# Optimization experiments

Hardware: AMD Instinct MI355X
Metric: run time of the kernel (lower is better)

Reference implementation:

```python
import jax, jax.numpy as jnp
import numpy as np
import math

B, T, C = 2, 2048, 1024
H = 16            # n_head
RATIO = 4         # ratio_kv
HKV = H // RATIO  # n_head_kv = 4
HD = C // H       # head_dim = 64
G = H // HKV      # query heads per kv head = 4


def _alibi_slopes(n_heads):
    # n_heads must be a power of 2 here (H=16)
    assert math.log2(n_heads).is_integer()
    start = 2.0 ** (-(2.0 ** (-(math.log2(n_heads) - 3))))
    return np.array([start * (start ** i) for i in range(n_heads)], dtype=np.float32)


def setup_inputs() -> dict:
    key = jax.random.key(0)
    ks = jax.random.split(key, 5)
    return {
        "x": jax.random.normal(ks[0], (B, T, C), dtype=jnp.float32),
        "Wq": jax.random.normal(ks[1], (C, C), dtype=jnp.float32) * 0.02,
        "Wk": jax.random.normal(ks[2], (C, HKV * HD), dtype=jnp.float32) * 0.02,
        "Wv": jax.random.normal(ks[3], (C, HKV * HD), dtype=jnp.float32) * 0.02,
        "Wo": jax.random.normal(ks[4], (C, C), dtype=jnp.float32) * 0.02,
    }


def reference(x, Wq, Wk, Wv, Wo):
    # GQA causal attention with ALiBi bias (flash-disabled fallback path).
    # q: [B,HKV,G,T,HD] (grouped query heads), k/v: [B,HKV,T,HD]
    q = (x @ Wq).reshape(B, T, H, HD).transpose(0, 2, 1, 3).reshape(B, HKV, G, T, HD)
    k = (x @ Wk).reshape(B, T, HKV, HD).transpose(0, 2, 1, 3)
    v = (x @ Wv).reshape(B, T, HKV, HD).transpose(0, 2, 1, 3)

    scale = 1.0 / math.sqrt(HD)
    att = jnp.einsum('bkgtd,bksd->bkgts', q, k) * scale  # [B,HKV,G,T,T]

    # ALiBi: original repeats alibi(n_head) by G and truncates to n_head,
    # so query head h uses slope get_slopes(H)[h // G] == slopes[:HKV] per kv group.
    slopes = jnp.asarray(_alibi_slopes(H))[:HKV]          # [HKV]
    pos = jnp.arange(T)
    rel = (pos[None, :] - pos[:, None]).astype(jnp.float32)  # [T,T], rel[i,j]=j-i
    bias = slopes[:, None, None] * rel                    # [HKV,T,T]
    causal = jnp.triu(jnp.full((T, T), -jnp.inf, dtype=jnp.float32), 1)

    att = att + bias[None, :, None] + causal
    att = jax.nn.softmax(att.astype(jnp.float32), axis=-1).astype(q.dtype)

    y = jnp.einsum('bkgts,bksd->bkgtd', att, v)           # [B,HKV,G,T,HD]
    y = y.reshape(B, H, T, HD).transpose(0, 2, 1, 3).reshape(B, T, C)
    return y @ Wo
```

## Files before the change

kernel.cpp:

```cpp
#include <hip/hip_runtime.h>
#include <hip/hip_bf16.h>
#include <math.h>

#define B_ 2
#define T_ 2048
#define C_ 1024
#define H_ 16
#define HKV_ 4
#define G_ 4
#define HD_ 64
#define KVC_ 256
#define NQKV_ 1536
#define NQT_ 32

typedef __attribute__((ext_vector_type(8))) short bf16x8;
typedef __attribute__((ext_vector_type(4))) float f32x4;

static __device__ inline short f2bf(float f) {
    __hip_bfloat16 h = __float2bfloat16(f);
    short s;
    __builtin_memcpy(&s, &h, 2);
    return s;
}
static __device__ inline short f2bf_trunc(float f) {
    unsigned int u;
    __builtin_memcpy(&u, &f, 4);
    return (short)(u >> 16);
}
static __device__ inline float bf2f(short s) {
    unsigned int u = ((unsigned int)(unsigned short)s) << 16;
    float f;
    __builtin_memcpy(&f, &u, 4);
    return f;
}

static __device__ inline void gload_lds16(const short* g, short* lds) {
    __builtin_amdgcn_global_load_lds(
        (const __attribute__((address_space(1))) unsigned int*)g,
        (__attribute__((address_space(3))) unsigned int*)lds, 16, 0, 0);
}

__global__ __launch_bounds__(256) void cast_bf16(
    const float* __restrict__ in, short* __restrict__ out, int n)
{
    const int i = (blockIdx.x * 256 + threadIdx.x) * 8;
    if (i >= n) return;
    const float4 a = *(const float4*)(in + i);
    const float4 b = *(const float4*)(in + i + 4);
    bf16x8 o;
    o[0] = f2bf(a.x); o[1] = f2bf(a.y); o[2] = f2bf(a.z); o[3] = f2bf(a.w);
    o[4] = f2bf(b.x); o[5] = f2bf(b.y); o[6] = f2bf(b.z); o[7] = f2bf(b.w);
    *(bf16x8*)(out + i) = o;
}

__global__ __launch_bounds__(256) void w_transpose(
    const float* __restrict__ Wq, const float* __restrict__ Wk,
    const float* __restrict__ Wv, const float* __restrict__ Wo,
    short* __restrict__ Wt, short* __restrict__ Wot)
{
    const int z = blockIdx.z;
    const float* in;
    short* out;
    int N;
    if (z == 0)      { in = Wq; out = Wt;                     N = C_; }
    else if (z == 1) { in = Wk; out = Wt + C_ * C_;           N = KVC_; }
    else if (z == 2) { in = Wv; out = Wt + (C_ + KVC_) * C_;  N = KVC_; }
    else             { in = Wo; out = Wot;                    N = C_; }
    const int n0 = blockIdx.x * 32;
    if (n0 >= N) return;
    __shared__ float t[32][33];
    const int tx = threadIdx.x, ty = threadIdx.y;
    const int k0 = blockIdx.y * 32;
    #pragma unroll
    for (int j = 0; j < 4; j++)
        t[ty + j * 8][tx] = in[(size_t)(k0 + ty + j * 8) * N + n0 + tx];
    __syncthreads();
    #pragma unroll
    for (int j = 0; j < 4; j++)
        out[(size_t)(n0 + ty + j * 8) * C_ + k0 + tx] = f2bf(t[tx][ty + j * 8]);
}

template <bool OUT_BF16>
__global__ __launch_bounds__(256) void gemm_bf16(
    const short* __restrict__ A, const short* __restrict__ Bt,
    void* __restrict__ Cout, int M, int N, int K)
{
    __shared__ short As[64 * 32];
    __shared__ short Bs[128 * 32];
    const int tid = threadIdx.x;
    const int wave = tid >> 6, lane = tid & 63;
    const int l15 = lane & 15, quad = lane >> 4;
    const int row0 = blockIdx.y * 64, col0 = blockIdx.x * 128;
    const int wrow = (wave >> 1) * 32, wcol = (wave & 1) * 64;

    f32x4 acc[2][4];
    #pragma unroll
    for (int i = 0; i < 2; i++)
        #pragma unroll
        for (int j = 0; j < 4; j++)
            acc[i][j] = (f32x4){0.f, 0.f, 0.f, 0.f};

    for (int kt = 0; kt < K; kt += 32) {
        __syncthreads();
        {
            const int r = wave * 16 + (lane >> 2);
            const int kof = (lane & 3) * 8;
            gload_lds16(A + (size_t)(row0 + r) * K + kt + kof, &As[wave * 512]);
        }
        #pragma unroll
        for (int c2 = 0; c2 < 2; c2++) {
            const int c = wave * 2 + c2;
            const int r = c * 16 + (lane >> 2);
            const int kof = (lane & 3) * 8;
            gload_lds16(Bt + (size_t)(col0 + r) * K + kt + kof, &Bs[c * 512]);
        }
        __syncthreads();

        bf16x8 af[2], bf[4];
        #pragma unroll
        for (int mt = 0; mt < 2; mt++)
            af[mt] = *(const bf16x8*)&As[(wrow + mt * 16 + l15) * 32 + quad * 8];
        #pragma unroll
        for (int nt = 0; nt < 4; nt++)
            bf[nt] = *(const bf16x8*)&Bs[(wcol + nt * 16 + l15) * 32 + quad * 8];
        #pragma unroll
        for (int mt = 0; mt < 2; mt++)
            #pragma unroll
            for (int nt = 0; nt < 4; nt++)
                acc[mt][nt] = __builtin_amdgcn_mfma_f32_16x16x32_bf16(
                    af[mt], bf[nt], acc[mt][nt], 0, 0, 0);
    }

    #pragma unroll
    for (int mt = 0; mt < 2; mt++) {
        #pragma unroll
        for (int r = 0; r < 4; r++) {
            const size_t row = row0 + wrow + mt * 16 + quad * 4 + r;
            #pragma unroll
            for (int nt = 0; nt < 4; nt++) {
                const size_t col = col0 + wcol + nt * 16 + l15;
                if (OUT_BF16)
                    ((short*)Cout)[row * N + col] = f2bf(acc[mt][nt][r]);
                else
                    ((float*)Cout)[row * N + col] = acc[mt][nt][r];
            }
        }
    }
}

__global__ __launch_bounds__(256) void kv_tile(
    const short* __restrict__ QKV, short* __restrict__ Kt, short* __restrict__ Vt)
{
    __shared__ short Ls[64 * 72];
    const int jt = blockIdx.x;
    const int bk = blockIdx.y;
    const int b = bk >> 2, kh = bk & 3;
    const int tid = threadIdx.x;
    const int key = tid >> 2, d16 = (tid & 3) * 16;
    const size_t src = (size_t)(b * T_ + jt * 64 + key) * NQKV_ + C_ + kh * 64 + d16;
    const size_t tbase = (size_t)(bk * 32 + jt) * 4096;

    {
        const int db0 = (tid & 3) * 2, db1 = db0 + 1;
        *(bf16x8*)(Kt + tbase + key * 64 + ((db0 ^ (key & 7)) * 8)) =
            *(const bf16x8*)(QKV + src);
        *(bf16x8*)(Kt + tbase + key * 64 + ((db1 ^ (key & 7)) * 8)) =
            *(const bf16x8*)(QKV + src + 8);
    }
    *(bf16x8*)&Ls[key * 72 + d16]     = *(const bf16x8*)(QKV + src + KVC_);
    *(bf16x8*)&Ls[key * 72 + d16 + 8] = *(const bf16x8*)(QKV + src + KVC_ + 8);
    __syncthreads();
    const int d = tid >> 2, k16 = (tid & 3) * 16;
    bf16x8 o0, o1;
    #pragma unroll
    for (int i = 0; i < 8; i++) o0[i] = Ls[(k16 + i) * 72 + d];
    #pragma unroll
    for (int i = 0; i < 8; i++) o1[i] = Ls[(k16 + 8 + i) * 72 + d];
    const int kb0 = (tid & 3) * 2, kb1 = kb0 + 1;
    *(bf16x8*)(Vt + tbase + d * 64 + ((kb0 ^ (d & 7)) * 8)) = o0;
    *(bf16x8*)(Vt + tbase + d * 64 + ((kb1 ^ (d & 7)) * 8)) = o1;
}

#define LSTR 72

__global__ __launch_bounds__(256) void attn_mfma(
    const short* __restrict__ QKV, const short* __restrict__ Ktg,
    const short* __restrict__ Vtg, short* __restrict__ Y)
{
    const int qx = blockIdx.x;
    const int bh = blockIdx.y;
    const int qtL = qx, qtH = NQT_ - 1 - qx;
    const int b = bh >> 4, h = bh & 15, kh = h >> 2;
    const float slope2 = exp2f(-0.5f * (float)(kh + 1)) * 1.44269504f;
    const int tid = threadIdx.x;
    const int wave = tid >> 6, lane = tid & 63;
    const int l15 = lane & 15, quad = lane >> 4;
    const int lswz = (l15 & 7) * 8;

    __shared__ short Ks[4096];
    __shared__ short Vs[4096];
    __shared__ short Ps[4 * 32 * LSTR];
    short* Pw = &Ps[wave * 32 * LSTR];
    const int wswz = ((quad >> 1) & 1) << 4;
    const int rswz = ((l15 >> 3) & 1) << 4;

    const size_t bT = (size_t)b * T_;
    const size_t tb0 = (size_t)((b * HKV_ + kh) * 32) * 4096;
    const int qrow0H = qtH * 64 + wave * 16;
    const int qrow0L = qtL * 64 + wave * 16;

    const float qscale = 0.125f * 1.44269504f;
    bf16x8 qfH[2], qfL[2];
    #pragma unroll
    for (int k0 = 0; k0 < 2; k0++) {
        const short* qpH = QKV + (bT + qrow0H + l15) * NQKV_ + h * 64;
        const short* qpL = QKV + (bT + qrow0L + l15) * NQKV_ + h * 64;
        bf16x8 rH = *(const bf16x8*)(qpH + k0 * 32 + quad * 8);
        bf16x8 rL = *(const bf16x8*)(qpL + k0 * 32 + quad * 8);
        #pragma unroll
        for (int j = 0; j < 8; j++) {
            qfH[k0][j] = f2bf(bf2f(rH[j]) * qscale);
            qfL[k0][j] = f2bf(bf2f(rL[j]) * qscale);
        }
    }

    const short one_s = (short)0x3F80;
    const bf16x8 ones = {one_s, one_s, one_s, one_s, one_s, one_s, one_s, one_s};

    f32x4 OaccH[4], OaccL[4], laccH, laccL;
    #pragma unroll
    for (int nt = 0; nt < 4; nt++) {
        OaccH[nt] = (f32x4){0.f, 0.f, 0.f, 0.f};
        OaccL[nt] = (f32x4){0.f, 0.f, 0.f, 0.f};
    }
    laccH = (f32x4){0.f, 0.f, 0.f, 0.f};
    laccL = (f32x4){0.f, 0.f, 0.f, 0.f};

    for (int jtk = 0; jtk <= qtH; jtk++) {
        __syncthreads();
        {
            const short* Ktile = Ktg + tb0 + (size_t)jtk * 4096;
            const short* Vtile = Vtg + tb0 + (size_t)jtk * 4096;
            #pragma unroll
            for (int i = 0; i < 2; i++) {
                const int ch = wave * 2 + i;
                gload_lds16(Ktile + ch * 512 + lane * 8, &Ks[ch * 512]);
                gload_lds16(Vtile + ch * 512 + lane * 8, &Vs[ch * 512]);
            }
        }
        __syncthreads();

        const bool doL = (jtk <= qtL);

        bf16x8 kf[8];
        #pragma unroll
        for (int nt = 0; nt < 4; nt++)
            #pragma unroll
            for (int k0 = 0; k0 < 2; k0++)
                kf[nt * 2 + k0] = *(const bf16x8*)
                    &Ks[(nt * 16 + l15) * 64 + (((k0 * 4 + quad) * 8) ^ lswz)];

        f32x4 sH[4], sL[4];
        #pragma unroll
        for (int nt = 0; nt < 4; nt++) {
            f32x4 a = {0.f, 0.f, 0.f, 0.f};
            a = __builtin_amdgcn_mfma_f32_16x16x32_bf16(qfH[0], kf[nt*2+0], a, 0, 0, 0);
            a = __builtin_amdgcn_mfma_f32_16x16x32_bf16(qfH[1], kf[nt*2+1], a, 0, 0, 0);
            sH[nt] = a;
        }
        if (doL) {
            #pragma unroll
            for (int nt = 0; nt < 4; nt++) {
                f32x4 a = {0.f, 0.f, 0.f, 0.f};
                a = __builtin_amdgcn_mfma_f32_16x16x32_bf16(qfL[0], kf[nt*2+0], a, 0, 0, 0);
                a = __builtin_amdgcn_mfma_f32_16x16x32_bf16(qfL[1], kf[nt*2+1], a, 0, 0, 0);
                sL[nt] = a;
            }
        }

        {
            const float base = slope2 * (float)(jtk * 64 + l15 - quad * 4 - qrow0H);
            if (jtk == qtH) {
                #pragma unroll
                for (int nt = 0; nt < 4; nt++) {
                    const int colsw = ((nt * 16 + l15) ^ wswz);
                    #pragma unroll
                    for (int r = 0; r < 4; r++) {
                        const float relv = (float)(jtk * 64 + l15 - quad * 4 - qrow0H)
                                         + (float)(nt * 16 - r);
                        float p = __builtin_amdgcn_exp2f(
                            fmaf(slope2, (float)(nt * 16 - r), base) + sH[nt][r]);
                        if (relv > 0.f) p = 0.f;
                        Pw[(quad * 4 + r) * LSTR + colsw] = f2bf_trunc(p);
                    }
                }
            } else {
                #pragma unroll
                for (int nt = 0; nt < 4; nt++) {
                    const int colsw = ((nt * 16 + l15) ^ wswz);
                    #pragma unroll
                    for (int r = 0; r < 4; r++) {
                        float p = __builtin_amdgcn_exp2f(
                            fmaf(slope2, (float)(nt * 16 - r), base) + sH[nt][r]);
                        Pw[(quad * 4 + r) * LSTR + colsw] = f2bf_trunc(p);
                    }
                }
            }
        }
        if (doL) {
            const float base = slope2 * (float)(jtk * 64 + l15 - quad * 4 - qrow0L);
            if (jtk == qtL) {
                #pragma unroll
                for (int nt = 0; nt < 4; nt++) {
                    const int colsw = ((nt * 16 + l15) ^ wswz);
                    #pragma unroll
                    for (int r = 0; r < 4; r++) {
                        const float relv = (float)(jtk * 64 + l15 - quad * 4 - qrow0L)
                                         + (float)(nt * 16 - r);
                        float p = __builtin_amdgcn_exp2f(
                            fmaf(slope2, (float)(nt * 16 - r), base) + sL[nt][r]);
                        if (relv > 0.f) p = 0.f;
                        Pw[(16 + quad * 4 + r) * LSTR + colsw] = f2bf_trunc(p);
                    }
                }
            } else {
                #pragma unroll
                for (int nt = 0; nt < 4; nt++) {
                    const int colsw = ((nt * 16 + l15) ^ wswz);
                    #pragma unroll
                    for (int r = 0; r < 4; r++) {
                        float p = __builtin_amdgcn_exp2f(
                            fmaf(slope2, (float)(nt * 16 - r), base) + sL[nt][r]);
                        Pw[(16 + quad * 4 + r) * LSTR + colsw] = f2bf_trunc(p);
                    }
                }
            }
        }
        __asm__ volatile("s_waitcnt lgkmcnt(0)" ::: "memory");

        bf16x8 vf[8];
        #pragma unroll
        for (int nt = 0; nt < 4; nt++)
            #pragma unroll
            for (int k0 = 0; k0 < 2; k0++)
                vf[nt * 2 + k0] = *(const bf16x8*)
                    &Vs[(nt * 16 + l15) * 64 + (((k0 * 4 + quad) * 8) ^ lswz)];

        {
            bf16x8 pf0 = *(const bf16x8*)&Pw[l15 * LSTR + ((quad * 8) ^ rswz)];
            bf16x8 pf1 = *(const bf16x8*)&Pw[l15 * LSTR + ((32 + quad * 8) ^ rswz)];
            laccH = __builtin_amdgcn_mfma_f32_16x16x32_bf16(pf0, ones, laccH, 0, 0, 0);
            laccH = __builtin_amdgcn_mfma_f32_16x16x32_bf16(pf1, ones, laccH, 0, 0, 0);
            #pragma unroll
            for (int nt = 0; nt < 4; nt++) {
                OaccH[nt] = __builtin_amdgcn_mfma_f32_16x16x32_bf16(
                    pf0, vf[nt*2+0], OaccH[nt], 0, 0, 0);
                OaccH[nt] = __builtin_amdgcn_mfma_f32_16x16x32_bf16(
                    pf1, vf[nt*2+1], OaccH[nt], 0, 0, 0);
            }
        }
        if (doL) {
            bf16x8 pf0 = *(const bf16x8*)&Pw[(16 + l15) * LSTR + ((quad * 8) ^ rswz)];
            bf16x8 pf1 = *(const bf16x8*)&Pw[(16 + l15) * LSTR + ((32 + quad * 8) ^ rswz)];
            laccL = __builtin_amdgcn_mfma_f32_16x16x32_bf16(pf0, ones, laccL, 0, 0, 0);
            laccL = __builtin_amdgcn_mfma_f32_16x16x32_bf16(pf1, ones, laccL, 0, 0, 0);
            #pragma unroll
            for (int nt = 0; nt < 4; nt++) {
                OaccL[nt] = __builtin_amdgcn_mfma_f32_16x16x32_bf16(
                    pf0, vf[nt*2+0], OaccL[nt], 0, 0, 0);
                OaccL[nt] = __builtin_amdgcn_mfma_f32_16x16x32_bf16(
                    pf1, vf[nt*2+1], OaccL[nt], 0, 0, 0);
            }
        }
    }

    #pragma unroll
    for (int r = 0; r < 4; r++) {
        const float invH = 1.f / laccH[r];
        const float invL = 1.f / laccL[r];
        const int rowH = qrow0H + quad * 4 + r;
        const int rowL = qrow0L + quad * 4 + r;
        short* ypH = Y + (bT + rowH) * C_ + h * 64 + l15;
        short* ypL = Y + (bT + rowL) * C_ + h * 64 + l15;
        #pragma unroll
        for (int nt = 0; nt < 4; nt++) {
            ypH[nt * 16] = f2bf(OaccH[nt][r] * invH);
            ypL[nt * 16] = f2bf(OaccL[nt][r] * invL);
        }
    }
}

extern "C" void kernel_launch(void* const* d_in, const int* in_sizes, int n_in,
                              void* d_out, int out_size, void* d_ws, size_t ws_size,
                              hipStream_t stream) {
    const float* x  = (const float*)d_in[0];
    const float* Wq = (const float*)d_in[1];
    const float* Wk = (const float*)d_in[2];
    const float* Wv = (const float*)d_in[3];
    const float* Wo = (const float*)d_in[4];
    float* out = (float*)d_out;

    const int M = B_ * T_;
    short* xb  = (short*)d_ws;
    short* Wt  = xb  + (size_t)M * C_;
    short* Wot = Wt  + (size_t)NQKV_ * C_;
    short* QKV = Wot + (size_t)C_ * C_;
    short* Yb  = QKV + (size_t)M * NQKV_;
    short* Ktg = Yb  + (size_t)M * C_;
    short* Vtg = Ktg + (size_t)8 * 32 * 4096;

    cast_bf16<<<dim3(M * C_ / (256 * 8)), dim3(256), 0, stream>>>(x, xb, M * C_);
    w_transpose<<<dim3(32, 32, 4), dim3(32, 8), 0, stream>>>(Wq, Wk, Wv, Wo, Wt, Wot);

    gemm_bf16<true><<<dim3(NQKV_ / 128, M / 64), dim3(256), 0, stream>>>(
        xb, Wt, QKV, M, NQKV_, C_);
    kv_tile<<<dim3(32, 8), dim3(256), 0, stream>>>(QKV, Ktg, Vtg);
    attn_mfma<<<dim3(NQT_ / 2, B_ * H_), dim3(256), 0, stream>>>(QKV, Ktg, Vtg, Yb);
    gemm_bf16<false><<<dim3(C_ / 128, M / 64), dim3(256), 0, stream>>>(
        Yb, Wot, out, M, C_, C_);
}
```

Baseline: 176.1 us.

## Fuse K/V tiling into QKV GEMM epilogue and keep P in registers

The QKV GEMM epilogue now writes K and V directly into the swizzled per-tile layouts the attention kernel expects, which removes the separate kv_tile kernel and its extra global round trip. In attention, scores are computed transposed (K·Q) with the ALiBi bias preloaded into the accumulator. P is packed into bf16x4 registers and fed to 16x16x16 MFMAs for both the row sums and the PV product, so the LDS P staging buffer and its waits are gone. The trade is more MFMA instructions at half the K depth and scattered 2-byte stores for K in the GEMM epilogue.

Measured after the change: 190.9 us. +8.4%, slower.

```diff
diff --git a/kernel.cpp b/kernel.cpp
--- a/kernel.cpp
+++ b/kernel.cpp
@@ -14,6 +14,7 @@
 #define NQT_ 32
 
 typedef __attribute__((ext_vector_type(8))) short bf16x8;
+typedef __attribute__((ext_vector_type(4))) short bf16x4;
 typedef __attribute__((ext_vector_type(4))) float f32x4;
 
 static __device__ inline short f2bf(float f) {
@@ -22,16 +23,27 @@
     __builtin_memcpy(&s, &h, 2);
     return s;
 }
-static __device__ inline short f2bf_trunc(float f) {
-    unsigned int u;
-    __builtin_memcpy(&u, &f, 4);
-    return (short)(u >> 16);
-}
 static __device__ inline float bf2f(short s) {
     unsigned int u = ((unsigned int)(unsigned short)s) << 16;
     float f;
     __builtin_memcpy(&f, &u, 4);
     return f;
+}
+static __device__ inline bf16x4 pack4_trunc(float p0, float p1, float p2, float p3) {
+    unsigned a, b, c, d;
+    __builtin_memcpy(&a, &p0, 4); __builtin_memcpy(&b, &p1, 4);
+    __builtin_memcpy(&c, &p2, 4); __builtin_memcpy(&d, &p3, 4);
+    int2 v;
+    v.x = (int)((a >> 16) | (b & 0xffff0000u));
+    v.y = (int)((c >> 16) | (d & 0xffff0000u));
+    return __builtin_bit_cast(bf16x4, v);
+}
+
+static __device__ inline f32x4 mfma32(bf16x8 a, bf16x8 b, f32x4 c) {
+    return __builtin_amdgcn_mfma_f32_16x16x32_bf16(a, b, c, 0, 0, 0);
+}
+static __device__ inline f32x4 mfma16(bf16x4 a, bf16x4 b, f32x4 c) {
+    return __builtin_amdgcn_mfma_f32_16x16x16bf16_1k(a, b, c, 0, 0, 0);
 }
 
 static __device__ inline void gload_lds16(const short* g, short* lds) {
@@ -80,10 +92,11 @@
         out[(size_t)(n0 + ty + j * 8) * C_ + k0 + tx] = f2bf(t[tx][ty + j * 8]);
 }
 
-template <bool OUT_BF16>
+template <int MODE>
 __global__ __launch_bounds__(256) void gemm_bf16(
     const short* __restrict__ A, const short* __restrict__ Bt,
-    void* __restrict__ Cout, int M, int N, int K)
+    void* __restrict__ Cout, short* __restrict__ Ktg, short* __restrict__ Vtg,
+    int M, int N, int K)
 {
     __shared__ short As[64 * 32];
     __shared__ short Bs[128 * 32];
@@ -127,61 +140,68 @@
         for (int mt = 0; mt < 2; mt++)
             #pragma unroll
             for (int nt = 0; nt < 4; nt++)
-                acc[mt][nt] = __builtin_amdgcn_mfma_f32_16x16x32_bf16(
-                    af[mt], bf[nt], acc[mt][nt], 0, 0, 0);
-    }
-
-    #pragma unroll
-    for (int mt = 0; mt < 2; mt++) {
-        #pragma unroll
-        for (int r = 0; r < 4; r++) {
-            const size_t row = row0 + wrow + mt * 16 + quad * 4 + r;
-            #pragma unroll
-            for (int nt = 0; nt < 4; nt++) {
-                const size_t col = col0 + wcol + nt * 16 + l15;
-                if (OUT_BF16)
-                    ((short*)Cout)[row * N + col] = f2bf(acc[mt][nt][r]);
-                else
-                    ((float*)Cout)[row * N + col] = acc[mt][nt][r];
-            }
-        }
-    }
-}
-
-__global__ __launch_bounds__(256) void kv_tile(
-    const short* __restrict__ QKV, short* __restrict__ Kt, short* __restrict__ Vt)
-{
-    __shared__ short Ls[64 * 72];
-    const int jt = blockIdx.x;
-    const int bk = blockIdx.y;
-    const int b = bk >> 2, kh = bk & 3;
-    const int tid = threadIdx.x;
-    const int key = tid >> 2, d16 = (tid & 3) * 16;
-    const size_t src = (size_t)(b * T_ + jt * 64 + key) * NQKV_ + C_ + kh * 64 + d16;
-    const size_t tbase = (size_t)(bk * 32 + jt) * 4096;
-
-    {
-        const int db0 = (tid & 3) * 2, db1 = db0 + 1;
-        *(bf16x8*)(Kt + tbase + key * 64 + ((db0 ^ (key & 7)) * 8)) =
-            *(const bf16x8*)(QKV + src);
-        *(bf16x8*)(Kt + tbase + key * 64 + ((db1 ^ (key & 7)) * 8)) =
-            *(const bf16x8*)(QKV + src + 8);
-    }
-    *(bf16x8*)&Ls[key * 72 + d16]     = *(const bf16x8*)(QKV + src + KVC_);
-    *(bf16x8*)&Ls[key * 72 + d16 + 8] = *(const bf16x8*)(QKV + src + KVC_ + 8);
-    __syncthreads();
-    const int d = tid >> 2, k16 = (tid & 3) * 16;
-    bf16x8 o0, o1;
-    #pragma unroll
-    for (int i = 0; i < 8; i++) o0[i] = Ls[(k16 + i) * 72 + d];
-    #pragma unroll
-    for (int i = 0; i < 8; i++) o1[i] = Ls[(k16 + 8 + i) * 72 + d];
-    const int kb0 = (tid & 3) * 2, kb1 = kb0 + 1;
-    *(bf16x8*)(Vt + tbase + d * 64 + ((kb0 ^ (d & 7)) * 8)) = o0;
-    *(bf16x8*)(Vt + tbase + d * 64 + ((kb1 ^ (d & 7)) * 8)) = o1;
-}
-
-#define LSTR 72
+                acc[mt][nt] = mfma32(af[mt], bf[nt], acc[mt][nt]);
+    }
+
+    if (MODE == 0) {
+        #pragma unroll
+        for (int mt = 0; mt < 2; mt++)
+            #pragma unroll
+            for (int r = 0; r < 4; r++) {
+                const size_t row = row0 + wrow + mt * 16 + quad * 4 + r;
+                #pragma unroll
+                for (int nt = 0; nt < 4; nt++)
+                    ((float*)Cout)[row * N + col0 + wcol + nt * 16 + l15]
+                        = acc[mt][nt][r];
+            }
+    } else {
+        if (col0 < C_) {
+            #pragma unroll
+            for (int mt = 0; mt < 2; mt++)
+                #pragma unroll
+                for (int r = 0; r < 4; r++) {
+                    const size_t row = row0 + wrow + mt * 16 + quad * 4 + r;
+                    #pragma unroll
+                    for (int nt = 0; nt < 4; nt++)
+                        ((short*)Cout)[row * N + col0 + wcol + nt * 16 + l15]
+                            = f2bf(acc[mt][nt][r]);
+                }
+        } else if (col0 < C_ + KVC_) {
+            const int kh = ((col0 - C_) >> 6) + (wcol >> 6);
+            const int b = row0 >> 11, jt = (row0 & (T_ - 1)) >> 6;
+            const size_t tbase = (size_t)((b * HKV_ + kh) * 32 + jt) * 4096;
+            #pragma unroll
+            for (int mt = 0; mt < 2; mt++)
+                #pragma unroll
+                for (int r = 0; r < 4; r++) {
+                    const int key = wrow + mt * 16 + quad * 4 + r;
+                    #pragma unroll
+                    for (int nt = 0; nt < 4; nt++) {
+                        const int d = nt * 16 + l15;
+                        Ktg[tbase + key * 64 + (((d >> 3) ^ (key & 7)) << 3) + (d & 7)]
+                            = f2bf(acc[mt][nt][r]);
+                    }
+                }
+        } else {
+            const int kh = ((col0 - C_ - KVC_) >> 6) + (wcol >> 6);
+            const int b = row0 >> 11, jt = (row0 & (T_ - 1)) >> 6;
+            const size_t tbase = (size_t)((b * HKV_ + kh) * 32 + jt) * 4096;
+            #pragma unroll
+            for (int mt = 0; mt < 2; mt++) {
+                const int kblk = ((wrow + mt * 16) >> 3) + (quad >> 1);
+                #pragma unroll
+                for (int nt = 0; nt < 4; nt++) {
+                    const int d = nt * 16 + l15;
+                    bf16x4 v4;
+                    v4[0] = f2bf(acc[mt][nt][0]); v4[1] = f2bf(acc[mt][nt][1]);
+                    v4[2] = f2bf(acc[mt][nt][2]); v4[3] = f2bf(acc[mt][nt][3]);
+                    *(bf16x4*)(Vtg + tbase + d * 64
+                               + ((kblk ^ (d & 7)) << 3) + ((quad & 1) << 2)) = v4;
+                }
+            }
+        }
+    }
+}
 
 __global__ __launch_bounds__(256) void attn_mfma(
     const short* __restrict__ QKV, const short* __restrict__ Ktg,
@@ -199,10 +219,6 @@
 
     __shared__ short Ks[4096];
     __shared__ short Vs[4096];
-    __shared__ short Ps[4 * 32 * LSTR];
-    short* Pw = &Ps[wave * 32 * LSTR];
-    const int wswz = ((quad >> 1) & 1) << 4;
-    const int rswz = ((l15 >> 3) & 1) << 4;
 
     const size_t bT = (size_t)b * T_;
     const size_t tb0 = (size_t)((b * HKV_ + kh) * 32) * 4096;
@@ -224,8 +240,18 @@
         }
     }
 
-    const short one_s = (short)0x3F80;
-    const bf16x8 ones = {one_s, one_s, one_s, one_s, one_s, one_s, one_s, one_s};
+    const float step = slope2 * 64.f;
+    f32x4 bBH[4], bBL[4];
+    #pragma unroll
+    for (int mtk = 0; mtk < 4; mtk++)
+        #pragma unroll
+        for (int r = 0; r < 4; r++) {
+            const int key0 = mtk * 16 + quad * 4 + r;
+            bBH[mtk][r] = slope2 * (float)(key0 - wave * 16 - l15 - qtH * 64);
+            bBL[mtk][r] = slope2 * (float)(key0 - wave * 16 - l15 - qtL * 64);
+        }
+
+    const bf16x4 ones = {(short)0x3F80, (short)0x3F80, (short)0x3F80, (short)0x3F80};
 
     f32x4 OaccH[4], OaccL[4], laccH, laccL;
     #pragma unroll
@@ -251,141 +277,83 @@
         __syncthreads();
 
         const bool doL = (jtk <= qtL);
+        const float jb = step * (float)jtk;
 
         bf16x8 kf[8];
         #pragma unroll
-        for (int nt = 0; nt < 4; nt++)
+        for (int mtk = 0; mtk < 4; mtk++)
             #pragma unroll
             for (int k0 = 0; k0 < 2; k0++)
-                kf[nt * 2 + k0] = *(const bf16x8*)
-                    &Ks[(nt * 16 + l15) * 64 + (((k0 * 4 + quad) * 8) ^ lswz)];
-
-        f32x4 sH[4], sL[4];
+                kf[mtk * 2 + k0] = *(const bf16x8*)
+                    &Ks[(mtk * 16 + l15) * 64 + (((k0 * 4 + quad) * 8) ^ lswz)];
+
+        bf16x4 pTH[4], pTL[4];
+        {
+            const bool diag = (jtk == qtH);
+            #pragma unroll
+            for (int mtk = 0; mtk < 4; mtk++) {
+                const f32x4 bias = bBH[mtk] + jb;
+                f32x4 a = bias;
+                a = mfma32(kf[mtk * 2 + 0], qfH[0], a);
+                a = mfma32(kf[mtk * 2 + 1], qfH[1], a);
+                float p[4];
+                #pragma unroll
+                for (int r = 0; r < 4; r++) {
+                    p[r] = __builtin_amdgcn_exp2f(a[r]);
+                    if (diag && bias[r] > 0.f) p[r] = 0.f;
+                }
+                pTH[mtk] = pack4_trunc(p[0], p[1], p[2], p[3]);
+                laccH = mfma16(ones, pTH[mtk], laccH);
+            }
+        }
+        if (doL) {
+            const bool diag = (jtk == qtL);
+            #pragma unroll
+            for (int mtk = 0; mtk < 4; mtk++) {
+                const f32x4 bias = bBL[mtk] + jb;
+                f32x4 a = bias;
+                a = mfma32(kf[mtk * 2 + 0], qfL[0], a);
+                a = mfma32(kf[mtk * 2 + 1], qfL[1], a);
+                float p[4];
+                #pragma unroll
+                for (int r = 0; r < 4; r++) {
+                    p[r] = __builtin_amdgcn_exp2f(a[r]);
+                    if (diag && bias[r] > 0.f) p[r] = 0.f;
+                }
+                pTL[mtk] = pack4_trunc(p[0], p[1], p[2], p[3]);
+                laccL = mfma16(ones, pTL[mtk], laccL);
+            }
+        }
+
+        #pragma unroll
+        for (int mtk = 0; mtk < 4; mtk++) {
+            const int kblk = (mtk << 1) + (quad >> 1);
+            #pragma unroll
+            for (int nt = 0; nt < 4; nt++) {
+                const bf16x4 vf = *(const bf16x4*)
+                    &Vs[(nt * 16 + l15) * 64
+                        + ((kblk ^ (l15 & 7)) << 3) + ((quad & 1) << 2)];
+                OaccH[nt] = mfma16(vf, pTH[mtk], OaccH[nt]);
+                if (doL) OaccL[nt] = mfma16(vf, pTL[mtk], OaccL[nt]);
+            }
+        }
+    }
+
+    {
+        const float invH = 1.f / laccH[0];
+        const float invL = 1.f / laccL[0];
+        short* ypH = Y + (bT + qrow0H + l15) * C_ + h * 64;
+        short* ypL = Y + (bT + qrow0L + l15) * C_ + h * 64;
         #pragma unroll
         for (int nt = 0; nt < 4; nt++) {
-            f32x4 a = {0.f, 0.f, 0.f, 0.f};
-            a = __builtin_amdgcn_mfma_f32_16x16x32_bf16(qfH[0], kf[nt*2+0], a, 0, 0, 0);
-            a = __builtin_amdgcn_mfma_f32_16x16x32_bf16(qfH[1], kf[nt*2+1], a, 0, 0, 0);
-            sH[nt] = a;
-        }
-        if (doL) {
-            #pragma unroll
-            for (int nt = 0; nt < 4; nt++) {
-                f32x4 a = {0.f, 0.f, 0.f, 0.f};
-                a = __builtin_amdgcn_mfma_f32_16x16x32_bf16(qfL[0], kf[nt*2+0], a, 0, 0, 0);
-                a = __builtin_amdgcn_mfma_f32_16x16x32_bf16(qfL[1], kf[nt*2+1], a, 0, 0, 0);
-                sL[nt] = a;
-            }
-        }
-
-        {
-            const float base = slope2 * (float)(jtk * 64 + l15 - quad * 4 - qrow0H);
-            if (jtk == qtH) {
-                #pragma unroll
-                for (int nt = 0; nt < 4; nt++) {
-                    const int colsw = ((nt * 16 + l15) ^ wswz);
-                    #pragma unroll
-                    for (int r = 0; r < 4; r++) {
-                        const float relv = (float)(jtk * 64 + l15 - quad * 4 - qrow0H)
-                                         + (float)(nt * 16 - r);
-                        float p = __builtin_amdgcn_exp2f(
-                            fmaf(slope2, (float)(nt * 16 - r), base) + sH[nt][r]);
-                        if (relv > 0.f) p = 0.f;
-                        Pw[(quad * 4 + r) * LSTR + colsw] = f2bf_trunc(p);
-                    }
-                }
-            } else {
-                #pragma unroll
-                for (int nt = 0; nt < 4; nt++) {
-                    const int colsw = ((nt * 16 + l15) ^ wswz);
-                    #pragma unroll
-                    for (int r = 0; r < 4; r++) {
-                        float p = __builtin_amdgcn_exp2f(
-                            fmaf(slope2, (float)(nt * 16 - r), base) + sH[nt][r]);
-                        Pw[(quad * 4 + r) * LSTR + colsw] = f2bf_trunc(p);
-                    }
-                }
-            }
-        }
-        if (doL) {
-            const float base = slope2 * (float)(jtk * 64 + l15 - quad * 4 - qrow0L);
-            if (jtk == qtL) {
-                #pragma unroll
-                for (int nt = 0; nt < 4; nt++) {
-                    const int colsw = ((nt * 16 + l15) ^ wswz);
-                    #pragma unroll
-                    for (int r = 0; r < 4; r++) {
-                        const float relv = (float)(jtk * 64 + l15 - quad * 4 - qrow0L)
-                                         + (float)(nt * 16 - r);
-                        float p = __builtin_amdgcn_exp2f(
-                            fmaf(slope2, (float)(nt * 16 - r), base) + sL[nt][r]);
-                        if (relv > 0.f) p = 0.f;
-                        Pw[(16 + quad * 4 + r) * LSTR + colsw] = f2bf_trunc(p);
-                    }
-                }
-            } else {
-                #pragma unroll
-                for (int nt = 0; nt < 4; nt++) {
-                    const int colsw = ((nt * 16 + l15) ^ wswz);
-                    #pragma unroll
-                    for (int r = 0; r < 4; r++) {
-                        float p = __builtin_amdgcn_exp2f(
-                            fmaf(slope2, (float)(nt * 16 - r), base) + sL[nt][r]);
-                        Pw[(16 + quad * 4 + r) * LSTR + colsw] = f2bf_trunc(p);
-                    }
-                }
-            }
-        }
-        __asm__ volatile("s_waitcnt lgkmcnt(0)" ::: "memory");
-
-        bf16x8 vf[8];
-        #pragma unroll
-        for (int nt = 0; nt < 4; nt++)
-            #pragma unroll
-            for (int k0 = 0; k0 < 2; k0++)
-                vf[nt * 2 + k0] = *(const bf16x8*)
-                    &Vs[(nt * 16 + l15) * 64 + (((k0 * 4 + quad) * 8) ^ lswz)];
-
-        {
-            bf16x8 pf0 = *(const bf16x8*)&Pw[l15 * LSTR + ((quad * 8) ^ rswz)];
-            bf16x8 pf1 = *(const bf16x8*)&Pw[l15 * LSTR + ((32 + quad * 8) ^ rswz)];
-            laccH = __builtin_amdgcn_mfma_f32_16x16x32_bf16(pf0, ones, laccH, 0, 0, 0);
-            laccH = __builtin_amdgcn_mfma_f32_16x16x32_bf16(pf1, ones, laccH, 0, 0, 0);
-            #pragma unroll
-            for (int nt = 0; nt < 4; nt++) {
-                OaccH[nt] = __builtin_amdgcn_mfma_f32_16x16x32_bf16(
-                    pf0, vf[nt*2+0], OaccH[nt], 0, 0, 0);
-                OaccH[nt] = __builtin_amdgcn_mfma_f32_16x16x32_bf16(
-                    pf1, vf[nt*2+1], OaccH[nt], 0, 0, 0);
-            }
-        }
-        if (doL) {
-            bf16x8 pf0 = *(const bf16x8*)&Pw[(16 + l15) * LSTR + ((quad * 8) ^ rswz)];
-            bf16x8 pf1 = *(const bf16x8*)&Pw[(16 + l15) * LSTR + ((32 + quad * 8) ^ rswz)];
-            laccL = __builtin_amdgcn_mfma_f32_16x16x32_bf16(pf0, ones, laccL, 0, 0, 0);
-            laccL = __builtin_amdgcn_mfma_f32_16x16x32_bf16(pf1, ones, laccL, 0, 0, 0);
-            #pragma unroll
-            for (int nt = 0; nt < 4; nt++) {
-                OaccL[nt] = __builtin_amdgcn_mfma_f32_16x16x32_bf16(
-                    pf0, vf[nt*2+0], OaccL[nt], 0, 0, 0);
-                OaccL[nt] = __builtin_amdgcn_mfma_f32_16x16x32_bf16(
-                    pf1, vf[nt*2+1], OaccL[nt], 0, 0, 0);
-            }
-        }
-    }
-
-    #pragma unroll
-    for (int r = 0; r < 4; r++) {
-        const float invH = 1.f / laccH[r];
-        const float invL = 1.f / laccL[r];
-        const int rowH = qrow0H + quad * 4 + r;
-        const int rowL = qrow0L + quad * 4 + r;
-        short* ypH = Y + (bT + rowH) * C_ + h * 64 + l15;
-        short* ypL = Y + (bT + rowL) * C_ + h * 64 + l15;
-        #pragma unroll
-        for (int nt = 0; nt < 4; nt++) {
-            ypH[nt * 16] = f2bf(OaccH[nt][r] * invH);
-            ypL[nt * 16] = f2bf(OaccL[nt][r] * invL);
+            bf16x4 oH, oL;
+            #pragma unroll
+            for (int r = 0; r < 4; r++) {
+                oH[r] = f2bf(OaccH[nt][r] * invH);
+                oL[r] = f2bf(OaccL[nt][r] * invL);
+            }
+            *(bf16x4*)(ypH + nt * 16 + quad * 4) = oH;
+            *(bf16x4*)(ypL + nt * 16 + quad * 4) = oL;
         }
     }
 }
@@ -412,10 +380,9 @@
     cast_bf16<<<dim3(M * C_ / (256 * 8)), dim3(256), 0, stream>>>(x, xb, M * C_);
     w_transpose<<<dim3(32, 32, 4), dim3(32, 8), 0, stream>>>(Wq, Wk, Wv, Wo, Wt, Wot);
 
-    gemm_bf16<true><<<dim3(NQKV_ / 128, M / 64), dim3(256), 0, stream>>>(
-        xb, Wt, QKV, M, NQKV_, C_);
-    kv_tile<<<dim3(32, 8), dim3(256), 0, stream>>>(QKV, Ktg, Vtg);
+    gemm_bf16<1><<<dim3(NQKV_ / 128, M / 64), dim3(256), 0, stream>>>(
+        xb, Wt, QKV, Ktg, Vtg, M, NQKV_, C_);
     attn_mfma<<<dim3(NQT_ / 2, B_ * H_), dim3(256), 0, stream>>>(QKV, Ktg, Vtg, Yb);
-    gemm_bf16<false><<<dim3(C_ / 128, M / 64), dim3(256), 0, stream>>>(
-        Yb, Wot, out, M, C_, C_);
-}
+    gemm_bf16<0><<<dim3(C_ / 128, M / 64), dim3(256), 0, stream>>>(
+        Yb, Wot, out, nullptr, nullptr, M, C_, C_);
+}
```
